# Kernel tuning notes

Hardware: AMD Instinct MI355X
Metric: run time of the kernel (lower is better)

Reference implementation:

```python
import jax, jax.numpy as jnp
import numpy as np

N = 100000   # nodes
E = 1600000  # edges
D = 128      # hidden_dim (also input feature dim)
R = 8        # num_relations
B = 4        # num_bases
OUT = 64     # out_dim
P = 2        # gating exponent p


def setup_inputs() -> dict:
    key = jax.random.key(0)
    ks = jax.random.split(key, 16)
    w = lambda k, shape, s=0.05: jax.random.normal(k, shape, dtype=jnp.float32) * s
    return {
        "x": jax.random.normal(ks[0], (N, D), dtype=jnp.float32),
        "src": jax.random.randint(ks[1], (E,), 0, N, dtype=jnp.int32),
        "dst": jax.random.randint(ks[2], (E,), 0, N, dtype=jnp.int32),
        "edge_type": jax.random.randint(ks[3], (E,), 0, R, dtype=jnp.int32),
        "proj_W": w(ks[4], (D, D)), "proj_b": jnp.zeros((D,), jnp.float32),
        "basis1": w(ks[5], (B, D, D)), "comp1": w(ks[6], (R, B), 1.0),
        "root1": w(ks[7], (D, D)), "bias1": jnp.zeros((D,), jnp.float32),
        "basis2": w(ks[8], (B, D, D)), "comp2": w(ks[9], (R, B), 1.0),
        "root2": w(ks[10], (D, D)), "bias2": jnp.zeros((D,), jnp.float32),
        "out_W": w(ks[11], (D, OUT)), "out_b": jnp.zeros((OUT,), jnp.float32),
    }


def _rgcn(x, src, dst, et, basis, comp, root, bias):
    # PyG RGCNConv (basis decomposition, aggr='mean'):
    # out_i = x_i @ root + bias + sum_r mean_{e: dst=i, type=r}( x_{src_e} @ W_r )
    # Mean is linear, so aggregate raw features per (node, relation), then matmul.
    n, d = x.shape
    seg = dst * R + et                                   # combined (node, relation) key
    agg = jax.ops.segment_sum(x[src], seg, num_segments=n * R).reshape(n, R, d)
    cnt = jax.ops.segment_sum(jnp.ones(seg.shape, x.dtype), seg, num_segments=n * R).reshape(n, R)
    agg = agg / jnp.maximum(cnt, 1.0)[:, :, None]        # empty segments -> 0
    W = jnp.einsum('rb,bdf->rdf', comp, basis)           # [R, D, D] relation weights
    return jnp.einsum('nrd,rdf->nf', agg, W) + x @ root + bias


def _gate(x, src, dst):
    # tau = tanh(scatter_mean(|x_src - x_dst|^p, index=src))
    diff = jnp.abs(x[src] - x[dst]) ** P                 # [E, D]
    s = jax.ops.segment_sum(diff, src, num_segments=x.shape[0])
    c = jax.ops.segment_sum(jnp.ones(src.shape, x.dtype), src, num_segments=x.shape[0])
    return jnp.tanh(s / jnp.maximum(c, 1.0)[:, None])


def reference(x, src, dst, edge_type, proj_W, proj_b,
              basis1, comp1, root1, bias1,
              basis2, comp2, root2, bias2,
              out_W, out_b):
    # input projection (dropout is identity in eval mode)
    h = jax.nn.relu(x @ proj_W + proj_b)
    latents = [h]
    for basis, comp, root, bias in ((basis1, comp1, root1, bias1),
                                    (basis2, comp2, root2, bias2)):
        h_new = jax.nn.relu(_rgcn(h, src, dst, edge_type, basis, comp, root, bias))
        tau = _gate(h, src, dst)
        h = (1.0 - tau) * h + tau * h_new
        latents.append(h)
    out = h @ out_W + out_b
    return (out, jnp.stack(latents))
```

## Files before the change

kernel.cpp:

```cpp
#include <hip/hip_runtime.h>
#include <cstdint>
#include <cstddef>

#define D 128
#define RR 8

typedef __attribute__((ext_vector_type(8))) short short8;
typedef __attribute__((ext_vector_type(4))) float f32x4;

__device__ inline ushort f2b(float x) {
    union { float f; unsigned u; } v; v.f = x;
    unsigned r = v.u + 0x7fff + ((v.u >> 16) & 1);
    return (ushort)(r >> 16);
}
__device__ inline float b2f(ushort u) {
    union { unsigned u; float f; } v; v.u = ((unsigned)u) << 16; return v.f;
}

__device__ inline void gload_lds16(const ushort* g, ushort* l) {
    __builtin_amdgcn_global_load_lds(
        (const __attribute__((address_space(1))) unsigned int*)g,
        (__attribute__((address_space(3))) unsigned int*)l, 16, 0, 0);
}

template<bool BIAS, bool RELU, bool STF, bool STB>
__global__ __launch_bounds__(256, 4) void gemm_bf16(
    const ushort* __restrict__ A0, int lda0, int k0steps,
    const ushort* __restrict__ A1, int lda1,
    const ushort* __restrict__ BT, int ktiles,
    const float* __restrict__ bias, float* __restrict__ Cf, int ldcf,
    ushort* __restrict__ Cb, int ldcb, int M, int ncol)
{
    __shared__ ushort As[128 * 64];
    __shared__ ushort Bs[128 * 64];
    const int tid = threadIdx.x;
    const int m0 = blockIdx.x * 128;
    const int ldb = ktiles * 128;
    const int ksteps = ktiles * 2;

    const int w = tid >> 6, lane = tid & 63;
    const int wm = (w & 1) * 64, wn = (w >> 1) * 64;
    const int l15 = lane & 15, quad = lane >> 4;

    const ushort* a0p[4];
    const ushort* a1p[4];
    const ushort* bp[4];
#pragma unroll
    for (int it = 0; it < 4; it++) {
        int gi = w * 256 + it * 64 + lane;
        int row = gi >> 3, g = gi & 7;
        int cg = g ^ (row & 7);
        int gr = m0 + row; if (gr > M - 1) gr = M - 1;
        a0p[it] = A0 + (size_t)gr * lda0 + (cg << 3);
        a1p[it] = A1 + (size_t)gr * lda1 + (cg << 3);
        bp[it]  = BT + (size_t)row * ldb + (cg << 3);
    }

    f32x4 acc[4][4];
    const f32x4 z4 = {0.f, 0.f, 0.f, 0.f};
#pragma unroll
    for (int i = 0; i < 4; i++)
#pragma unroll
        for (int j = 0; j < 4; j++) acc[i][j] = z4;

    for (int kt = 0; kt < ksteps; kt++) {
        const int ko = kt * 64;
        if (kt < k0steps) {
#pragma unroll
            for (int it = 0; it < 4; it++)
                gload_lds16(a0p[it] + ko, As + w * 2048 + it * 512);
        } else {
            const int ko1 = (kt - k0steps) * 64;
#pragma unroll
            for (int it = 0; it < 4; it++)
                gload_lds16(a1p[it] + ko1, As + w * 2048 + it * 512);
        }
#pragma unroll
        for (int it = 0; it < 4; it++)
            gload_lds16(bp[it] + ko, Bs + w * 2048 + it * 512);
        __syncthreads();

#pragma unroll
        for (int ks = 0; ks < 64; ks += 32) {
            const int q0 = (ks >> 3) + quad;
            short8 af[4], bfr[4];
#pragma unroll
            for (int i = 0; i < 4; i++) {
                int row = wm + i * 16 + l15;
                af[i] = *(const short8*)(&As[row * 64 + ((q0 ^ (row & 7)) << 3)]);
            }
#pragma unroll
            for (int j = 0; j < 4; j++) {
                int row = wn + j * 16 + l15;
                bfr[j] = *(const short8*)(&Bs[row * 64 + ((q0 ^ (row & 7)) << 3)]);
            }
#pragma unroll
            for (int i = 0; i < 4; i++)
#pragma unroll
                for (int j = 0; j < 4; j++)
                    acc[i][j] = __builtin_amdgcn_mfma_f32_16x16x32_bf16(
                        af[i], bfr[j], acc[i][j], 0, 0, 0);
        }
        __syncthreads();
    }

#pragma unroll
    for (int i = 0; i < 4; i++) {
#pragma unroll
        for (int q = 0; q < 4; q++) {
            int gm = m0 + wm + i * 16 + quad * 4 + q;
            if (gm >= M) continue;
#pragma unroll
            for (int j = 0; j < 4; j++) {
                int gn = wn + j * 16 + l15;
                if (gn >= ncol) continue;
                float v = acc[i][j][q];
                if (BIAS) v += bias[gn];
                if (RELU) v = v > 0.f ? v : 0.f;
                if (STF) Cf[(size_t)gm * ldcf + gn] = v;
                if (STB) Cb[(size_t)gm * ldcb + gn] = f2b(v);
            }
        }
    }
}

__global__ void build_bigBT(const float* __restrict__ basis,
                            const float* __restrict__ comp,
                            const float* __restrict__ root,
                            ushort* __restrict__ BT)
{
    int i = blockIdx.x * 256 + threadIdx.x;
    if (i >= 128 * 1152) return;
    int f = i / 1152, c = i - f * 1152;
    float a;
    if (c < 1024) {
        int r = c >> 7, d = c & 127;
        a = 0.f;
#pragma unroll
        for (int b = 0; b < 4; b++)
            a += comp[r * 4 + b] * basis[(b * 128 + d) * 128 + f];
    } else {
        a = root[(c - 1024) * 128 + f];
    }
    BT[i] = f2b(a);
}

__global__ void transpose_pad(const float* __restrict__ in, ushort* __restrict__ out,
                              int cols)
{
    int i = blockIdx.x * 256 + threadIdx.x;
    if (i >= 128 * 128) return;
    int k = i & 127, f = i >> 7;
    out[i] = (f < cols) ? f2b(in[k * cols + f]) : (ushort)0;
}

__global__ void cast_x(const float* __restrict__ in, ushort* __restrict__ Hc, int total4)
{
    int i = blockIdx.x * 256 + threadIdx.x;
    if (i >= total4) return;
    float4 v = ((const float4*)in)[i];
    ushort4 o = { f2b(v.x), f2b(v.y), f2b(v.z), f2b(v.w) };
    *(ushort4*)(Hc + (size_t)i * 4) = o;
}

__global__ void count_edges(const int* __restrict__ src, const int* __restrict__ dst,
                            const int* __restrict__ et, int* __restrict__ cnt,
                            int* __restrict__ deg, int E)
{
    int e0 = (blockIdx.x * 256 + threadIdx.x) * 4;
#pragma unroll
    for (int j = 0; j < 4; j++) {
        int e = e0 + j;
        if (e < E) {
            atomicAdd(&cnt[dst[e] * RR + et[e]], 1);
            atomicAdd(&deg[src[e]], 1);
        }
    }
}

__global__ void scan1(const int* __restrict__ in, int* __restrict__ bsum, int n)
{
    __shared__ int s[256];
    const int b = blockIdx.x, t = threadIdx.x;
    const int base = b * 1024;
    int v = 0;
#pragma unroll
    for (int i = 0; i < 4; i++) {
        int idx = base + t * 4 + i;
        if (idx < n) v += in[idx];
    }
    s[t] = v; __syncthreads();
    for (int off = 128; off > 0; off >>= 1) {
        if (t < off) s[t] += s[t + off];
        __syncthreads();
    }
    if (t == 0) bsum[b] = s[0];
}

__global__ void scan_top(int* __restrict__ bsum, int nb)
{
    __shared__ int s[1024];
    const int t = threadIdx.x;
    int v = (t < nb) ? bsum[t] : 0;
    s[t] = v; __syncthreads();
    for (int off = 1; off < 1024; off <<= 1) {
        int x = (t >= off) ? s[t - off] : 0;
        __syncthreads();
        s[t] += x;
        __syncthreads();
    }
    if (t < nb) bsum[t] = s[t] - v;
}

__global__ void scan2(const int* __restrict__ in, const int* __restrict__ bsum,
                      int* __restrict__ out, int n)
{
    __shared__ int s[256];
    const int b = blockIdx.x, t = threadIdx.x;
    const int base = b * 1024;
    int loc[4];
    int v = 0;
#pragma unroll
    for (int i = 0; i < 4; i++) {
        int idx = base + t * 4 + i;
        int x = (idx < n) ? in[idx] : 0;
        loc[i] = v; v += x;
    }
    s[t] = v; __syncthreads();
    for (int off = 1; off < 256; off <<= 1) {
        int x = (t >= off) ? s[t - off] : 0;
        __syncthreads();
        s[t] += x;
        __syncthreads();
    }
    const int add = bsum[b] + (s[t] - v);
#pragma unroll
    for (int i = 0; i < 4; i++) {
        int idx = base + t * 4 + i;
        if (idx < n) out[idx] = add + loc[i];
    }
}

__global__ void fill_both(const int* __restrict__ src, const int* __restrict__ dst,
                          const int* __restrict__ et,
                          const int* __restrict__ aoff, int* __restrict__ acur,
                          int* __restrict__ acsr,
                          const int* __restrict__ goff, int* __restrict__ gcur,
                          int* __restrict__ gcsr, int E)
{
    int e0 = (blockIdx.x * 256 + threadIdx.x) * 4;
#pragma unroll
    for (int j = 0; j < 4; j++) {
        int e = e0 + j;
        if (e < E) {
            int s0 = src[e], d0 = dst[e];
            int seg = d0 * RR + et[e];
            int p = aoff[seg] + atomicAdd(&acur[seg], 1);
            acsr[p] = s0;
            int pg = goff[s0] + atomicAdd(&gcur[s0], 1);
            gcsr[pg] = d0;
        }
    }
}

__global__ __launch_bounds__(256) void gate_gather(
    const ushort* __restrict__ Hc, const int* __restrict__ gcsr,
    const int* __restrict__ goff, const int* __restrict__ deg,
    ushort* __restrict__ TAUb, int N)
{
    const int g = threadIdx.x >> 4, lane = threadIdx.x & 15;
    const int n = blockIdx.x * 16 + g;
    if (n >= N) return;
    const int start = goff[n];
    const int c = deg[n];
    const ushort* hbase = Hc + lane * 8;
    const short8 a8 = *(const short8*)(hbase + (size_t)n * 128);
    float av[8];
#pragma unroll
    for (int j = 0; j < 8; j++) av[j] = b2f((ushort)a8[j]);
    float acc[8];
#pragma unroll
    for (int j = 0; j < 8; j++) acc[j] = 0.f;

    int i = 0;
    for (; i + 4 <= c; i += 4) {
        int d0 = gcsr[start + i],     d1 = gcsr[start + i + 1];
        int d2 = gcsr[start + i + 2], d3 = gcsr[start + i + 3];
        short8 b0 = *(const short8*)(hbase + (size_t)d0 * 128);
        short8 b1 = *(const short8*)(hbase + (size_t)d1 * 128);
        short8 b2 = *(const short8*)(hbase + (size_t)d2 * 128);
        short8 b3 = *(const short8*)(hbase + (size_t)d3 * 128);
#pragma unroll
        for (int j = 0; j < 8; j++) {
            float dx0 = av[j] - b2f((ushort)b0[j]);
            float dx1 = av[j] - b2f((ushort)b1[j]);
            float dx2 = av[j] - b2f((ushort)b2[j]);
            float dx3 = av[j] - b2f((ushort)b3[j]);
            acc[j] += dx0 * dx0 + dx1 * dx1 + dx2 * dx2 + dx3 * dx3;
        }
    }
    if (i + 2 <= c) {
        int d0 = gcsr[start + i], d1 = gcsr[start + i + 1];
        short8 b0 = *(const short8*)(hbase + (size_t)d0 * 128);
        short8 b1 = *(const short8*)(hbase + (size_t)d1 * 128);
#pragma unroll
        for (int j = 0; j < 8; j++) {
            float dx0 = av[j] - b2f((ushort)b0[j]);
            float dx1 = av[j] - b2f((ushort)b1[j]);
            acc[j] += dx0 * dx0 + dx1 * dx1;
        }
        i += 2;
    }
    if (i < c) {
        int d0 = gcsr[start + i];
        short8 b0 = *(const short8*)(hbase + (size_t)d0 * 128);
#pragma unroll
        for (int j = 0; j < 8; j++) {
            float dx0 = av[j] - b2f((ushort)b0[j]);
            acc[j] += dx0 * dx0;
        }
    }
    const float inv = (c > 0) ? (1.f / (float)c) : 1.f;
    short8 t;
#pragma unroll
    for (int j = 0; j < 8; j++) t[j] = (short)f2b(tanhf(acc[j] * inv));
    *(short8*)(TAUb + (size_t)n * D + lane * 8) = t;
}

__global__ __launch_bounds__(256) void agg_gather(
    ushort* __restrict__ Agg, const ushort* __restrict__ Hc,
    const int* __restrict__ acsr, const int* __restrict__ aoff,
    const int* __restrict__ cnt, int N)
{
    const int g = threadIdx.x >> 4, lane = threadIdx.x & 15;
    const int n = blockIdx.x * 16 + g;
    if (n >= N) return;
    const int sbase = n * RR;
    int idx = aoff[sbase];
    const ushort* hbase = Hc + lane * 8;
    ushort* obase = Agg + (size_t)n * 1024 + lane * 8;

    for (int r = 0; r < RR; r++) {
        const int c = cnt[sbase + r];
        short8 outv = {0, 0, 0, 0, 0, 0, 0, 0};
        if (c > 0) {
            float acc[8];
#pragma unroll
            for (int j = 0; j < 8; j++) acc[j] = 0.f;
            int i = 0;
            for (; i + 4 <= c; i += 4) {
                int s0 = acsr[idx + i],     s1 = acsr[idx + i + 1];
                int s2 = acsr[idx + i + 2], s3 = acsr[idx + i + 3];
                short8 y0 = *(const short8*)(hbase + (size_t)s0 * 128);
                short8 y1 = *(const short8*)(hbase + (size_t)s1 * 128);
                short8 y2 = *(const short8*)(hbase + (size_t)s2 * 128);
                short8 y3 = *(const short8*)(hbase + (size_t)s3 * 128);
#pragma unroll
                for (int j = 0; j < 8; j++)
                    acc[j] += (b2f((ushort)y0[j]) + b2f((ushort)y1[j]))
                            + (b2f((ushort)y2[j]) + b2f((ushort)y3[j]));
            }
            if (i + 2 <= c) {
                int s0 = acsr[idx + i], s1 = acsr[idx + i + 1];
                short8 y0 = *(const short8*)(hbase + (size_t)s0 * 128);
                short8 y1 = *(const short8*)(hbase + (size_t)s1 * 128);
#pragma unroll
                for (int j = 0; j < 8; j++)
                    acc[j] += b2f((ushort)y0[j]) + b2f((ushort)y1[j]);
                i += 2;
            }
            if (i < c) {
                int s0 = acsr[idx + i];
                short8 y0 = *(const short8*)(hbase + (size_t)s0 * 128);
#pragma unroll
                for (int j = 0; j < 8; j++)
                    acc[j] += b2f((ushort)y0[j]);
            }
            const float inv = 1.f / (float)c;
#pragma unroll
            for (int j = 0; j < 8; j++) outv[j] = (short)f2b(acc[j] * inv);
            idx += c;
        }
        __builtin_nontemporal_store(outv, (short8*)(obase + r * 128));
    }
}

__global__ void finalize(const float* __restrict__ hp, float* __restrict__ hn,
                         const ushort* __restrict__ TAUb, ushort* __restrict__ Hc,
                         int total4)
{
    int idx = blockIdx.x * 256 + threadIdx.x;
    if (idx >= total4) return;
    const float4 p = ((const float4*)hp)[idx];
    const float4 a = ((const float4*)hn)[idx];
    const ushort4 t4 = ((const ushort4*)TAUb)[idx];
    float4 o;
    o.x = p.x + b2f(t4.x) * (a.x - p.x);
    o.y = p.y + b2f(t4.y) * (a.y - p.y);
    o.z = p.z + b2f(t4.z) * (a.z - p.z);
    o.w = p.w + b2f(t4.w) * (a.w - p.w);
    ((float4*)hn)[idx] = o;
    ushort4 ob = { f2b(o.x), f2b(o.y), f2b(o.z), f2b(o.w) };
    *(ushort4*)(Hc + (size_t)idx * 4) = ob;
}

extern "C" void kernel_launch(void* const* d_in, const int* in_sizes, int n_in,
                              void* d_out, int out_size, void* d_ws, size_t ws_size,
                              hipStream_t stream)
{
    const float* x      = (const float*)d_in[0];
    const int*   src    = (const int*)  d_in[1];
    const int*   dst    = (const int*)  d_in[2];
    const int*   etyp   = (const int*)  d_in[3];
    const float* projW  = (const float*)d_in[4];
    const float* projb  = (const float*)d_in[5];
    const float* basis1 = (const float*)d_in[6];
    const float* comp1  = (const float*)d_in[7];
    const float* root1  = (const float*)d_in[8];
    const float* bias1  = (const float*)d_in[9];
    const float* basis2 = (const float*)d_in[10];
    const float* comp2  = (const float*)d_in[11];
    const float* root2  = (const float*)d_in[12];
    const float* bias2  = (const float*)d_in[13];
    const float* outW   = (const float*)d_in[14];
    const float* outb   = (const float*)d_in[15];

    const int N    = in_sizes[0] / D;
    const int E    = in_sizes[1];
    const int OUTD = in_sizes[15];

    float* out  = (float*)d_out;
    float* lat0 = out + (size_t)N * OUTD;
    float* lat1 = lat0 + (size_t)N * D;
    float* lat2 = lat1 + (size_t)N * D;

    char* p = (char*)d_ws;
    ushort* Agg   = (ushort*)p;  p += (size_t)N * 1024 * 2;
    ushort* Hc    = (ushort*)p;  p += (size_t)N * 128 * 2;
    ushort* TAUb  = (ushort*)p;  p += (size_t)N * D * 2;
    ushort* projWT = (ushort*)p; p += 16384 * 2;
    ushort* outWT  = (ushort*)p; p += 16384 * 2;
    ushort* bigBT1 = (ushort*)p; p += (size_t)128 * 1152 * 2;
    ushort* bigBT2 = (ushort*)p; p += (size_t)128 * 1152 * 2;
    int* cnt_i  = (int*)p;       p += (size_t)N * RR * 4;
    int* deg_i  = (int*)p;       p += (size_t)N * 4;
    int* acur   = (int*)p;       p += (size_t)N * RR * 4;
    int* gcur   = (int*)p;       p += (size_t)N * 4;
    int* aoff   = (int*)p;       p += (size_t)N * RR * 4;
    int* goff   = (int*)p;       p += (size_t)N * 4;
    int* acsr   = (int*)p;       p += (size_t)E * 4;
    int* gcsr   = (int*)p;       p += (size_t)E * 4;
    int* bsum   = (int*)p;       p += 4096;

    if ((size_t)(p - (char*)d_ws) > ws_size) return;

    hipMemsetAsync(cnt_i, 0, sizeof(int) * 2 * ((size_t)N * RR + N), stream);

    build_bigBT<<<(128 * 1152 + 255) / 256, 256, 0, stream>>>(basis1, comp1, root1, bigBT1);
    build_bigBT<<<(128 * 1152 + 255) / 256, 256, 0, stream>>>(basis2, comp2, root2, bigBT2);
    transpose_pad<<<64, 256, 0, stream>>>(projW, projWT, 128);
    transpose_pad<<<64, 256, 0, stream>>>(outW, outWT, OUTD);

    cast_x<<<(N * 32 + 255) / 256, 256, 0, stream>>>(x, Hc, N * 32);

    count_edges<<<(E / 4 + 255) / 256, 256, 0, stream>>>(src, dst, etyp, cnt_i, deg_i, E);

    {
        int n1 = N * RR, nb1 = (n1 + 1023) / 1024;
        scan1<<<nb1, 256, 0, stream>>>(cnt_i, bsum, n1);
        scan_top<<<1, 1024, 0, stream>>>(bsum, nb1);
        scan2<<<nb1, 256, 0, stream>>>(cnt_i, bsum, aoff, n1);
        int nb2 = (N + 1023) / 1024;
        scan1<<<nb2, 256, 0, stream>>>(deg_i, bsum, N);
        scan_top<<<1, 1024, 0, stream>>>(bsum, nb2);
        scan2<<<nb2, 256, 0, stream>>>(deg_i, bsum, goff, N);
    }

    fill_both<<<(E / 4 + 255) / 256, 256, 0, stream>>>(
        src, dst, etyp, aoff, acur, acsr, goff, gcur, gcsr, E);

    const int mb = (N + 127) / 128;
    const int nodeblocks16 = (N + 15) / 16;

    gemm_bf16<true, true, true, true><<<mb, 256, 0, stream>>>(
        Hc, 128, 2, Hc, 128, projWT, 1, projb, lat0, 128, Hc, 128, N, 128);

    const ushort* bigBT[2] = {bigBT1, bigBT2};
    const float* biases[2] = {bias1, bias2};
    float* lats[3]         = {lat0, lat1, lat2};

    for (int l = 0; l < 2; l++) {
        float* hn = lats[l + 1];

        gate_gather<<<nodeblocks16, 256, 0, stream>>>(Hc, gcsr, goff, deg_i, TAUb, N);
        agg_gather<<<nodeblocks16, 256, 0, stream>>>(Agg, Hc, acsr, aoff, cnt_i, N);

        gemm_bf16<true, true, true, false><<<mb, 256, 0, stream>>>(
            Agg, 1024, 16, Hc, 128, bigBT[l], 9, biases[l], hn, 128, nullptr, 0, N, 128);

        finalize<<<(N * 32 + 255) / 256, 256, 0, stream>>>(
            lats[l], hn, TAUb, Hc, N * 32);
    }

    gemm_bf16<true, false, true, false><<<mb, 256, 0, stream>>>(
        Hc, 128, 2, Hc, 128, outWT, 1, outb, out, OUTD, nullptr, 0, N, OUTD);
}
```

Before: 1.120 ms.

## Record atomic slots in counting pass and flatten per-relation aggregation loop

The counting kernel now saves the atomicAdd return value per edge as its slot, so the fill pass scatters directly without a second round of atomics or cursor arrays, and the cursor memset shrinks. Each edge's slot is written to and read back from two new E-sized arrays. Separately, agg_gather now walks all of a node's incoming edges in one unrolled loop using running prefix sums and flushes a relation mean at each segment boundary, instead of running a separate short loop per relation. This keeps memory loads in flight across relation boundaries but computes each mean as a difference of cumulative sums, which adds float rounding error and extra branching inside the loop.

```diff
diff --git a/kernel.cpp b/kernel.cpp
--- a/kernel.cpp
+++ b/kernel.cpp
@@ -163,17 +163,18 @@
     *(ushort4*)(Hc + (size_t)i * 4) = o;
 }
 
-__global__ void count_edges(const int* __restrict__ src, const int* __restrict__ dst,
-                            const int* __restrict__ et, int* __restrict__ cnt,
-                            int* __restrict__ deg, int E)
+__global__ void count_slot(const int* __restrict__ src, const int* __restrict__ dst,
+                           const int* __restrict__ et, int* __restrict__ cnt,
+                           int* __restrict__ deg, int* __restrict__ slotA,
+                           int* __restrict__ slotG, int E)
 {
     int e0 = (blockIdx.x * 256 + threadIdx.x) * 4;
 #pragma unroll
     for (int j = 0; j < 4; j++) {
         int e = e0 + j;
         if (e < E) {
-            atomicAdd(&cnt[dst[e] * RR + et[e]], 1);
-            atomicAdd(&deg[src[e]], 1);
+            slotA[e] = atomicAdd(&cnt[dst[e] * RR + et[e]], 1);
+            slotG[e] = atomicAdd(&deg[src[e]], 1);
         }
     }
 }
@@ -241,12 +242,11 @@
     }
 }
 
-__global__ void fill_both(const int* __restrict__ src, const int* __restrict__ dst,
-                          const int* __restrict__ et,
-                          const int* __restrict__ aoff, int* __restrict__ acur,
-                          int* __restrict__ acsr,
-                          const int* __restrict__ goff, int* __restrict__ gcur,
-                          int* __restrict__ gcsr, int E)
+__global__ void fill_scatter(const int* __restrict__ src, const int* __restrict__ dst,
+                             const int* __restrict__ et,
+                             const int* __restrict__ aoff, const int* __restrict__ goff,
+                             const int* __restrict__ slotA, const int* __restrict__ slotG,
+                             int* __restrict__ acsr, int* __restrict__ gcsr, int E)
 {
     int e0 = (blockIdx.x * 256 + threadIdx.x) * 4;
 #pragma unroll
@@ -254,11 +254,8 @@
         int e = e0 + j;
         if (e < E) {
             int s0 = src[e], d0 = dst[e];
-            int seg = d0 * RR + et[e];
-            int p = aoff[seg] + atomicAdd(&acur[seg], 1);
-            acsr[p] = s0;
-            int pg = goff[s0] + atomicAdd(&gcur[s0], 1);
-            gcsr[pg] = d0;
+            acsr[aoff[d0 * RR + et[e]] + slotA[e]] = s0;
+            gcsr[goff[s0] + slotG[e]] = d0;
         }
     }
 }
@@ -336,53 +333,67 @@
     const int n = blockIdx.x * 16 + g;
     if (n >= N) return;
     const int sbase = n * RR;
-    int idx = aoff[sbase];
+    const int start = aoff[sbase];
+    int ctot = 0;
+#pragma unroll
+    for (int r0 = 0; r0 < RR; r0++) ctot += cnt[sbase + r0];
+
     const ushort* hbase = Hc + lane * 8;
     ushort* obase = Agg + (size_t)n * 1024 + lane * 8;
 
-    for (int r = 0; r < RR; r++) {
-        const int c = cnt[sbase + r];
+    float cum[8], prev[8];
+#pragma unroll
+    for (int j = 0; j < 8; j++) { cum[j] = 0.f; prev[j] = 0.f; }
+    int r = 0;
+    int segstart = 0;
+    int nexte = cnt[sbase];
+
+    auto flush = [&]() {
+        int c = nexte - segstart;
         short8 outv = {0, 0, 0, 0, 0, 0, 0, 0};
         if (c > 0) {
-            float acc[8];
-#pragma unroll
-            for (int j = 0; j < 8; j++) acc[j] = 0.f;
-            int i = 0;
-            for (; i + 4 <= c; i += 4) {
-                int s0 = acsr[idx + i],     s1 = acsr[idx + i + 1];
-                int s2 = acsr[idx + i + 2], s3 = acsr[idx + i + 3];
-                short8 y0 = *(const short8*)(hbase + (size_t)s0 * 128);
-                short8 y1 = *(const short8*)(hbase + (size_t)s1 * 128);
-                short8 y2 = *(const short8*)(hbase + (size_t)s2 * 128);
-                short8 y3 = *(const short8*)(hbase + (size_t)s3 * 128);
-#pragma unroll
-                for (int j = 0; j < 8; j++)
-                    acc[j] += (b2f((ushort)y0[j]) + b2f((ushort)y1[j]))
-                            + (b2f((ushort)y2[j]) + b2f((ushort)y3[j]));
-            }
-            if (i + 2 <= c) {
-                int s0 = acsr[idx + i], s1 = acsr[idx + i + 1];
-                short8 y0 = *(const short8*)(hbase + (size_t)s0 * 128);
-                short8 y1 = *(const short8*)(hbase + (size_t)s1 * 128);
-#pragma unroll
-                for (int j = 0; j < 8; j++)
-                    acc[j] += b2f((ushort)y0[j]) + b2f((ushort)y1[j]);
-                i += 2;
-            }
-            if (i < c) {
-                int s0 = acsr[idx + i];
-                short8 y0 = *(const short8*)(hbase + (size_t)s0 * 128);
-#pragma unroll
-                for (int j = 0; j < 8; j++)
-                    acc[j] += b2f((ushort)y0[j]);
-            }
-            const float inv = 1.f / (float)c;
-#pragma unroll
-            for (int j = 0; j < 8; j++) outv[j] = (short)f2b(acc[j] * inv);
-            idx += c;
+            float inv = 1.f / (float)c;
+#pragma unroll
+            for (int j = 0; j < 8; j++)
+                outv[j] = (short)f2b((cum[j] - prev[j]) * inv);
         }
         __builtin_nontemporal_store(outv, (short8*)(obase + r * 128));
-    }
+#pragma unroll
+        for (int j = 0; j < 8; j++) prev[j] = cum[j];
+        segstart = nexte;
+        r++;
+        if (r < RR) nexte += cnt[sbase + r];
+    };
+
+    int i = 0;
+    for (; i + 4 <= ctot; i += 4) {
+        int s0 = acsr[start + i],     s1 = acsr[start + i + 1];
+        int s2 = acsr[start + i + 2], s3 = acsr[start + i + 3];
+        short8 y0 = *(const short8*)(hbase + (size_t)s0 * 128);
+        short8 y1 = *(const short8*)(hbase + (size_t)s1 * 128);
+        short8 y2 = *(const short8*)(hbase + (size_t)s2 * 128);
+        short8 y3 = *(const short8*)(hbase + (size_t)s3 * 128);
+        while (i >= nexte) flush();
+#pragma unroll
+        for (int j = 0; j < 8; j++) cum[j] += b2f((ushort)y0[j]);
+        while (i + 1 >= nexte) flush();
+#pragma unroll
+        for (int j = 0; j < 8; j++) cum[j] += b2f((ushort)y1[j]);
+        while (i + 2 >= nexte) flush();
+#pragma unroll
+        for (int j = 0; j < 8; j++) cum[j] += b2f((ushort)y2[j]);
+        while (i + 3 >= nexte) flush();
+#pragma unroll
+        for (int j = 0; j < 8; j++) cum[j] += b2f((ushort)y3[j]);
+    }
+    for (; i < ctot; i++) {
+        int s0 = acsr[start + i];
+        short8 y0 = *(const short8*)(hbase + (size_t)s0 * 128);
+        while (i >= nexte) flush();
+#pragma unroll
+        for (int j = 0; j < 8; j++) cum[j] += b2f((ushort)y0[j]);
+    }
+    while (r < RR) flush();
 }
 
 __global__ void finalize(const float* __restrict__ hp, float* __restrict__ hn,
@@ -444,17 +455,17 @@
     ushort* bigBT2 = (ushort*)p; p += (size_t)128 * 1152 * 2;
     int* cnt_i  = (int*)p;       p += (size_t)N * RR * 4;
     int* deg_i  = (int*)p;       p += (size_t)N * 4;
-    int* acur   = (int*)p;       p += (size_t)N * RR * 4;
-    int* gcur   = (int*)p;       p += (size_t)N * 4;
     int* aoff   = (int*)p;       p += (size_t)N * RR * 4;
     int* goff   = (int*)p;       p += (size_t)N * 4;
+    int* slotA  = (int*)p;       p += (size_t)E * 4;
+    int* slotG  = (int*)p;       p += (size_t)E * 4;
     int* acsr   = (int*)p;       p += (size_t)E * 4;
     int* gcsr   = (int*)p;       p += (size_t)E * 4;
     int* bsum   = (int*)p;       p += 4096;
 
     if ((size_t)(p - (char*)d_ws) > ws_size) return;
 
-    hipMemsetAsync(cnt_i, 0, sizeof(int) * 2 * ((size_t)N * RR + N), stream);
+    hipMemsetAsync(cnt_i, 0, sizeof(int) * ((size_t)N * RR + N), stream);
 
     build_bigBT<<<(128 * 1152 + 255) / 256, 256, 0, stream>>>(basis1, comp1, root1, bigBT1);
     build_bigBT<<<(128 * 1152 + 255) / 256, 256, 0, stream>>>(basis2, comp2, root2, bigBT2);
@@ -463,7 +474,8 @@
 
     cast_x<<<(N * 32 + 255) / 256, 256, 0, stream>>>(x, Hc, N * 32);
 
-    count_edges<<<(E / 4 + 255) / 256, 256, 0, stream>>>(src, dst, etyp, cnt_i, deg_i, E);
+    count_slot<<<(E / 4 + 255) / 256, 256, 0, stream>>>(
+        src, dst, etyp, cnt_i, deg_i, slotA, slotG, E);
 
     {
         int n1 = N * RR, nb1 = (n1 + 1023) / 1024;
@@ -476,8 +488,8 @@
         scan2<<<nb2, 256, 0, stream>>>(deg_i, bsum, goff, N);
     }
 
-    fill_both<<<(E / 4 + 255) / 256, 256, 0, stream>>>(
-        src, dst, etyp, aoff, acur, acsr, goff, gcur, gcsr, E);
+    fill_scatter<<<(E / 4 + 255) / 256, 256, 0, stream>>>(
+        src, dst, etyp, aoff, goff, slotA, slotG, acsr, gcsr, E);
 
     const int mb = (N + 127) / 128;
     const int nodeblocks16 = (N + 15) / 16;
```

Result: faster. 1.051 ms (-6.2%).
